# Kernel tuning notes

Hardware: AMD Instinct MI355X
Metric: run time of the kernel (lower is better)

Reference implementation:

```python
import jax, jax.numpy as jnp
import numpy as np

N, E, G = 100000, 800000, 1
DV, DE, DU, H = 64, 32, 32, 128

def _w(key, shape):
    return jax.random.normal(key, shape, dtype=jnp.float32) * 0.05

def setup_inputs() -> dict:
    key = jax.random.key(0)
    ks = jax.random.split(key, 16)
    inp = {
        "node_attr": jax.random.normal(ks[0], (N, DV), dtype=jnp.float32),
        "edges": jax.random.randint(ks[1], (2, E), 0, N, dtype=jnp.int64 if jax.config.jax_enable_x64 else jnp.int32),
        "edge_attr": jax.random.normal(ks[2], (E, DE), dtype=jnp.float32),
        "u": jax.random.normal(ks[3], (G, DU), dtype=jnp.float32),
        "node_idx": jnp.zeros((N,), dtype=jnp.int32),
        "edge_idx": jnp.zeros((E,), dtype=jnp.int32),
        # edge MLP: concat(src, dst, edge_attr, u) -> H -> H
        "W1e": _w(ks[4], (2 * DV + DE + DU, H)), "b1e": jnp.zeros((H,), jnp.float32),
        "W2e": _w(ks[5], (H, H)), "b2e": jnp.zeros((H,), jnp.float32),
        # node MLP: concat(node_attr, aggregated_edges, u) -> H -> H
        "W1n": _w(ks[6], (DV + H + DU, H)), "b1n": jnp.zeros((H,), jnp.float32),
        "W2n": _w(ks[7], (H, H)), "b2n": jnp.zeros((H,), jnp.float32),
        # global MLP: concat(node_mean, edge_mean, u) -> H -> H
        "W1g": _w(ks[8], (H + H + DU, H)), "b1g": jnp.zeros((H,), jnp.float32),
        "W2g": _w(ks[9], (H, H)), "b2g": jnp.zeros((H,), jnp.float32),
    }
    return inp

def _mlp(x, W1, b1, W2, b2):
    return jax.nn.relu(x @ W1 + b1) @ W2 + b2

def _seg_mean(x, seg, num):
    s = jax.ops.segment_sum(x, seg, num_segments=num)
    c = jax.ops.segment_sum(jnp.ones((x.shape[0], 1), x.dtype), seg, num_segments=num)
    return s / jnp.maximum(c, 1.0)

def reference(node_attr, edges, edge_attr, u, node_idx, edge_idx,
              W1e, b1e, W2e, b2e, W1n, b1n, W2n, b2n, W1g, b1g, W2g, b2g):
    row, col = edges[0], edges[1]
    # edge model: gather endpoint features, concat with edge/global attrs
    e_in = jnp.concatenate([node_attr[row], node_attr[col], edge_attr, u[edge_idx]], axis=-1)
    e = _mlp(e_in, W1e, b1e, W2e, b2e)                        # [E, H]
    # node model: scatter-add incoming edge messages onto receivers (col)
    agg = jax.ops.segment_sum(e, col, num_segments=node_attr.shape[0])  # [N, H]
    v_in = jnp.concatenate([node_attr, agg, u[node_idx]], axis=-1)
    v = _mlp(v_in, W1n, b1n, W2n, b2n)                        # [N, H]
    # global model: per-graph mean pooling of nodes and edges
    nv = _seg_mean(v, node_idx, u.shape[0])                   # [G, H]
    ne = _seg_mean(e, edge_idx, u.shape[0])                   # [G, H]
    g_in = jnp.concatenate([nv, ne, u], axis=-1)
    g = _mlp(g_in, W1g, b1g, W2g, b2g)                        # [G, H]
    return v, e, g
```

## Files before the change

### kernel.cpp

```cpp
#include <hip/hip_runtime.h>

#define N_NODES 100000
#define N_EDGES 800000
#define DV 64
#define DE 32
#define DU 32
#define H 128

#define NTILES_E (N_EDGES / 64)

typedef short bf16x8 __attribute__((ext_vector_type(8)));
typedef unsigned short u16;
typedef u16 u16x8 __attribute__((ext_vector_type(8)));
typedef float f32x4 __attribute__((ext_vector_type(4)));

#define OFF_ESUM 0
#define OFF_VSUM 8192
#define OFF_BIAS 16384
#define OFF_PART 17408
#define OFF_WBUF 19456
#define OFF_DEG  175104
#define OFF_OFFS 575104
#define OFF_BUCK 975104

#define W1ET_OFF 0
#define W2ET_OFF 20480
#define W1NT_OFF 36864
#define W2NT_OFF 61440
#define WBUF_ELEMS 77824

#define NPART 391

__device__ inline u16 f2bf(float x) {
  union { float f; unsigned u; } c; c.f = x;
  unsigned r = c.u + 0x7FFFu + ((c.u >> 16) & 1u);
  return (u16)(r >> 16);
}

__global__ void prep_weights(const float* __restrict__ W1e, const float* __restrict__ W2e,
                             const float* __restrict__ W1n, const float* __restrict__ W2n,
                             u16* __restrict__ wbuf) {
  int i = blockIdx.x * blockDim.x + threadIdx.x;
  if (i < 20480) {
    int j = i / 160, k = i - j * 160;
    wbuf[W1ET_OFF + i] = f2bf(W1e[k * H + j]);
  } else if (i < 36864) {
    int t = i - 20480; int j = t >> 7, k = t & 127;
    wbuf[i] = f2bf(W2e[k * H + j]);
  } else if (i < 61440) {
    int t = i - 36864; int j = t / 192, k = t - j * 192;
    wbuf[i] = f2bf(W1n[k * H + j]);
  } else if (i < WBUF_ELEMS) {
    int t = i - 61440; int j = t >> 7, k = t & 127;
    wbuf[i] = f2bf(W2n[k * H + j]);
  }
}

__global__ void prep_bias(const float* __restrict__ uattr,
                          const float* __restrict__ W1e, const float* __restrict__ b1e,
                          const float* __restrict__ W1n, const float* __restrict__ b1n,
                          float* __restrict__ bias) {
  int t = threadIdx.x;
  float be = b1e[t];
  float bn = b1n[t];
  for (int k = 0; k < DU; ++k) {
    float uk = uattr[k];
    be += uk * W1e[(2 * DV + DE + k) * H + t];
    bn += uk * W1n[(DV + H + k) * H + t];
  }
  bias[t] = be;
  bias[128 + t] = bn;
}

__global__ void degree_kernel(const int* __restrict__ edges, int* __restrict__ deg) {
  int i = blockIdx.x * 256 + threadIdx.x;
  if (i < N_EDGES) atomicAdd(&deg[edges[N_EDGES + i]], 1);
}

__global__ void scan_part(const int* __restrict__ deg, int* __restrict__ part) {
  int i = blockIdx.x * 256 + threadIdx.x;
  int v = (i < N_NODES) ? deg[i] : 0;
#pragma unroll
  for (int m = 1; m < 64; m <<= 1) v += __shfl_xor(v, m);
  __shared__ int s[4];
  if ((threadIdx.x & 63) == 0) s[threadIdx.x >> 6] = v;
  __syncthreads();
  if (threadIdx.x == 0) part[blockIdx.x] = s[0] + s[1] + s[2] + s[3];
}

__global__ void scan_top(int* __restrict__ part) {
  __shared__ int s[512];
  int t = threadIdx.x;
  s[t] = (t < NPART) ? part[t] : 0;
  __syncthreads();
  for (int d = 1; d < 512; d <<= 1) {
    int v = (t >= d) ? s[t - d] : 0;
    __syncthreads();
    s[t] += v;
    __syncthreads();
  }
  if (t < NPART) part[t] = (t == 0) ? 0 : s[t - 1];
}

__global__ void scan_down(const int* __restrict__ part, int* __restrict__ deg_cursor,
                          int* __restrict__ offsets) {
  __shared__ int s[256];
  int b = blockIdx.x, t = threadIdx.x;
  int i = b * 256 + t;
  int v = (i < N_NODES) ? deg_cursor[i] : 0;
  s[t] = v;
  __syncthreads();
  for (int d = 1; d < 256; d <<= 1) {
    int u = (t >= d) ? s[t - d] : 0;
    __syncthreads();
    s[t] += u;
    __syncthreads();
  }
  int excl = s[t] - v + part[b];
  if (i < N_NODES) { offsets[i] = excl; deg_cursor[i] = excl; }
}

__global__ void fill_kernel(const int* __restrict__ edges, int* __restrict__ cursor,
                            int* __restrict__ bucket) {
  int i = blockIdx.x * 256 + threadIdx.x;
  if (i < N_EDGES) {
    int d = edges[N_EDGES + i];
    int pos = atomicAdd(&cursor[d], 1);
    bucket[pos] = i;
  }
}

__global__ __launch_bounds__(256, 3) void edge_kernel(
    const float* __restrict__ node_attr, const int* __restrict__ edges,
    const float* __restrict__ edge_attr,
    const u16* __restrict__ wbuf, const float* __restrict__ bias_f,
    const float* __restrict__ b2,
    float* __restrict__ e_out, float* __restrict__ esum_p)
{
  __shared__ __align__(16) u16 Hs[64][132];

  const int tid = threadIdx.x;
  const int wave = tid >> 6, lane = tid & 63;
  const int l15 = lane & 15, lg = lane >> 4;
  const int kc = lg * 8;
  const int wc = wave * 32;
  const long e0 = (long)blockIdx.x * 64;

  bf16x8 w1[5][2];
  {
    const u16* w1t = wbuf + W1ET_OFF;
#pragma unroll
    for (int cf = 0; cf < 2; ++cf) {
      const u16* p1 = w1t + (wc + cf * 16 + l15) * 160 + kc;
#pragma unroll
      for (int ks = 0; ks < 5; ++ks) w1[ks][cf] = *(const bf16x8*)(p1 + ks * 32);
    }
  }
  float bias1[2] = { bias_f[wc + l15], bias_f[wc + 16 + l15] };

  int sid[4], did[4];
#pragma unroll
  for (int rf = 0; rf < 4; ++rf) {
    sid[rf] = edges[e0 + rf * 16 + l15];
    did[rf] = edges[(long)N_EDGES + e0 + rf * 16 + l15];
  }

  f32x4 acc[4][2];
#pragma unroll
  for (int rf = 0; rf < 4; ++rf)
#pragma unroll
    for (int cf = 0; cf < 2; ++cf)
#pragma unroll
      for (int j = 0; j < 4; ++j) acc[rf][cf][j] = 0.f;

#pragma unroll
  for (int ks = 0; ks < 5; ++ks) {
    f32x4 ga[4], gb[4];
#pragma unroll
    for (int rf = 0; rf < 4; ++rf) {
      const float* p;
      if (ks == 0)      p = node_attr + (long)sid[rf] * DV + kc;
      else if (ks == 1) p = node_attr + (long)sid[rf] * DV + 32 + kc;
      else if (ks == 2) p = node_attr + (long)did[rf] * DV + kc;
      else if (ks == 3) p = node_attr + (long)did[rf] * DV + 32 + kc;
      else              p = edge_attr + (e0 + rf * 16 + l15) * DE + kc;
      ga[rf] = *(const f32x4*)p;
      gb[rf] = *(const f32x4*)(p + 4);
    }
#pragma unroll
    for (int rf = 0; rf < 4; ++rf) {
      u16x8 a;
      a[0] = f2bf(ga[rf][0]); a[1] = f2bf(ga[rf][1]);
      a[2] = f2bf(ga[rf][2]); a[3] = f2bf(ga[rf][3]);
      a[4] = f2bf(gb[rf][0]); a[5] = f2bf(gb[rf][1]);
      a[6] = f2bf(gb[rf][2]); a[7] = f2bf(gb[rf][3]);
      acc[rf][0] = __builtin_amdgcn_mfma_f32_16x16x32_bf16((bf16x8)a, w1[ks][0], acc[rf][0], 0, 0, 0);
      acc[rf][1] = __builtin_amdgcn_mfma_f32_16x16x32_bf16((bf16x8)a, w1[ks][1], acc[rf][1], 0, 0, 0);
    }
  }

#pragma unroll
  for (int rf = 0; rf < 4; ++rf)
#pragma unroll
    for (int cf = 0; cf < 2; ++cf)
#pragma unroll
      for (int j = 0; j < 4; ++j) {
        float hv = acc[rf][cf][j] + bias1[cf];
        hv = hv > 0.f ? hv : 0.f;
        Hs[rf * 16 + lg * 4 + j][wc + cf * 16 + l15] = f2bf(hv);
      }

  bf16x8 w2[4][2];
  {
    const u16* w2t = wbuf + W2ET_OFF;
#pragma unroll
    for (int cf = 0; cf < 2; ++cf) {
      const u16* p2 = w2t + (wc + cf * 16 + l15) * 128 + kc;
#pragma unroll
      for (int ks = 0; ks < 4; ++ks) w2[ks][cf] = *(const bf16x8*)(p2 + ks * 32);
    }
  }
  float bias2[2] = { b2[wc + l15], b2[wc + 16 + l15] };

  __syncthreads();

#pragma unroll
  for (int rf = 0; rf < 4; ++rf)
#pragma unroll
    for (int cf = 0; cf < 2; ++cf)
#pragma unroll
      for (int j = 0; j < 4; ++j) acc[rf][cf][j] = 0.f;

#pragma unroll
  for (int ks = 0; ks < 4; ++ks) {
#pragma unroll
    for (int rf = 0; rf < 4; ++rf) {
      bf16x8 a = *(const bf16x8*)&Hs[rf * 16 + l15][ks * 32 + kc];
      acc[rf][0] = __builtin_amdgcn_mfma_f32_16x16x32_bf16(a, w2[ks][0], acc[rf][0], 0, 0, 0);
      acc[rf][1] = __builtin_amdgcn_mfma_f32_16x16x32_bf16(a, w2[ks][1], acc[rf][1], 0, 0, 0);
    }
  }

  float es0 = 0.f, es1 = 0.f;
#pragma unroll
  for (int rf = 0; rf < 4; ++rf) {
#pragma unroll
    for (int cf = 0; cf < 2; ++cf) {
      int colg = wc + cf * 16 + l15;
#pragma unroll
      for (int j = 0; j < 4; ++j) {
        float v = acc[rf][cf][j] + bias2[cf];
        long r = rf * 16 + lg * 4 + j;
        e_out[(e0 + r) * H + colg] = v;
        if (cf == 0) es0 += v; else es1 += v;
      }
    }
  }

#pragma unroll
  for (int m = 16; m < 64; m <<= 1) { es0 += __shfl_xor(es0, m); es1 += __shfl_xor(es1, m); }
  if (lane < 16) {
    atomicAdd(&esum_p[(wc + lane) * 16], es0);
    atomicAdd(&esum_p[(wc + 16 + lane) * 16], es1);
  }
}

__global__ __launch_bounds__(512, 2) void node_kernel(
    const float* __restrict__ node_attr, const u16* __restrict__ wbuf,
    const float* __restrict__ bias_f, const float* __restrict__ b2,
    const float* __restrict__ e_out, const int* __restrict__ offsets,
    const int* __restrict__ cursor, const int* __restrict__ bucket,
    float* __restrict__ v_out, float* __restrict__ vsum_p)
{
  __shared__ __align__(16) u16 X[64][196];
  __shared__ __align__(16) u16 Hs[64][132];

  const int tid = threadIdx.x;
  const int wave = tid >> 6, lane = tid & 63;
  const int l15 = lane & 15, lg = lane >> 4;
  const int wc = (wave & 3) * 32;
  const int rh = (wave >> 2) * 32;
  const long n0 = (long)blockIdx.x * 64;

  {
    int gr = tid >> 3, gs = tid & 7;
    long gn = n0 + gr; if (gn >= N_NODES) gn = N_NODES - 1;
    float a[16];
#pragma unroll
    for (int k = 0; k < 16; ++k) a[k] = 0.f;
    int s = offsets[gn], e = cursor[gn];
    int i = s;
    for (; i + 2 <= e; i += 2) {
      const float* p0 = e_out + (long)bucket[i] * H + gs * 16;
      const float* p1 = e_out + (long)bucket[i + 1] * H + gs * 16;
      float4 f0[4], f1[4];
#pragma unroll
      for (int k = 0; k < 4; ++k) f0[k] = *(const float4*)(p0 + k * 4);
#pragma unroll
      for (int k = 0; k < 4; ++k) f1[k] = *(const float4*)(p1 + k * 4);
#pragma unroll
      for (int k = 0; k < 4; ++k) {
        a[k * 4 + 0] += f0[k].x + f1[k].x;
        a[k * 4 + 1] += f0[k].y + f1[k].y;
        a[k * 4 + 2] += f0[k].z + f1[k].z;
        a[k * 4 + 3] += f0[k].w + f1[k].w;
      }
    }
    if (i < e) {
      const float* p0 = e_out + (long)bucket[i] * H + gs * 16;
#pragma unroll
      for (int k = 0; k < 4; ++k) {
        float4 f = *(const float4*)(p0 + k * 4);
        a[k * 4 + 0] += f.x; a[k * 4 + 1] += f.y;
        a[k * 4 + 2] += f.z; a[k * 4 + 3] += f.w;
      }
    }
#pragma unroll
    for (int k = 0; k < 2; ++k) {
      u16x8 pk;
#pragma unroll
      for (int j = 0; j < 8; ++j) pk[j] = f2bf(a[k * 8 + j]);
      *(u16x8*)&X[gr][64 + gs * 16 + k * 8] = pk;
    }
  }

  {
    int r = tid >> 3, col = (tid & 7) * 8;
    long n = n0 + r; if (n >= N_NODES) n = N_NODES - 1;
    const float* src = node_attr + n * DV + col;
    float4 f0 = *(const float4*)src;
    float4 f1 = *(const float4*)(src + 4);
    u16x8 p;
    p[0] = f2bf(f0.x); p[1] = f2bf(f0.y); p[2] = f2bf(f0.z); p[3] = f2bf(f0.w);
    p[4] = f2bf(f1.x); p[5] = f2bf(f1.y); p[6] = f2bf(f1.z); p[7] = f2bf(f1.w);
    *(u16x8*)&X[r][col] = p;
  }

  bf16x8 w1[6][2], w2[4][2];
  {
    const u16* w1t = wbuf + W1NT_OFF;
    const u16* w2t = wbuf + W2NT_OFF;
#pragma unroll
    for (int cf = 0; cf < 2; ++cf) {
      const u16* p1 = w1t + (wc + cf * 16 + l15) * 192 + lg * 8;
#pragma unroll
      for (int ks = 0; ks < 6; ++ks) w1[ks][cf] = *(const bf16x8*)(p1 + ks * 32);
      const u16* p2 = w2t + (wc + cf * 16 + l15) * 128 + lg * 8;
#pragma unroll
      for (int ks = 0; ks < 4; ++ks) w2[ks][cf] = *(const bf16x8*)(p2 + ks * 32);
    }
  }

  __syncthreads();

  f32x4 acc[2][2];
#pragma unroll
  for (int rf = 0; rf < 2; ++rf)
#pragma unroll
    for (int cf = 0; cf < 2; ++cf)
#pragma unroll
      for (int j = 0; j < 4; ++j) acc[rf][cf][j] = 0.f;

#pragma unroll
  for (int ks = 0; ks < 6; ++ks) {
#pragma unroll
    for (int rf = 0; rf < 2; ++rf) {
      bf16x8 a = *(const bf16x8*)&X[rh + rf * 16 + l15][ks * 32 + lg * 8];
      acc[rf][0] = __builtin_amdgcn_mfma_f32_16x16x32_bf16(a, w1[ks][0], acc[rf][0], 0, 0, 0);
      acc[rf][1] = __builtin_amdgcn_mfma_f32_16x16x32_bf16(a, w1[ks][1], acc[rf][1], 0, 0, 0);
    }
  }

  float bias1[2] = { bias_f[128 + wc + l15], bias_f[128 + wc + 16 + l15] };
#pragma unroll
  for (int rf = 0; rf < 2; ++rf)
#pragma unroll
    for (int cf = 0; cf < 2; ++cf)
#pragma unroll
      for (int j = 0; j < 4; ++j) {
        float hv = acc[rf][cf][j] + bias1[cf];
        hv = hv > 0.f ? hv : 0.f;
        Hs[rh + rf * 16 + lg * 4 + j][wc + cf * 16 + l15] = f2bf(hv);
      }

  __syncthreads();

#pragma unroll
  for (int rf = 0; rf < 2; ++rf)
#pragma unroll
    for (int cf = 0; cf < 2; ++cf)
#pragma unroll
      for (int j = 0; j < 4; ++j) acc[rf][cf][j] = 0.f;

#pragma unroll
  for (int ks = 0; ks < 4; ++ks) {
#pragma unroll
    for (int rf = 0; rf < 2; ++rf) {
      bf16x8 a = *(const bf16x8*)&Hs[rh + rf * 16 + l15][ks * 32 + lg * 8];
      acc[rf][0] = __builtin_amdgcn_mfma_f32_16x16x32_bf16(a, w2[ks][0], acc[rf][0], 0, 0, 0);
      acc[rf][1] = __builtin_amdgcn_mfma_f32_16x16x32_bf16(a, w2[ks][1], acc[rf][1], 0, 0, 0);
    }
  }

  float bias2[2] = { b2[wc + l15], b2[wc + 16 + l15] };
  float vs0 = 0.f, vs1 = 0.f;
#pragma unroll
  for (int rf = 0; rf < 2; ++rf) {
#pragma unroll
    for (int cf = 0; cf < 2; ++cf) {
      int colg = wc + cf * 16 + l15;
#pragma unroll
      for (int j = 0; j < 4; ++j) {
        int r = rh + rf * 16 + lg * 4 + j;
        long n = n0 + r;
        if (n < N_NODES) {
          float v = acc[rf][cf][j] + bias2[cf];
          v_out[n * H + colg] = v;
          if (cf == 0) vs0 += v; else vs1 += v;
        }
      }
    }
  }
#pragma unroll
  for (int m = 16; m < 64; m <<= 1) { vs0 += __shfl_xor(vs0, m); vs1 += __shfl_xor(vs1, m); }
  if (lane < 16) {
    atomicAdd(&vsum_p[(wc + lane) * 16], vs0);
    atomicAdd(&vsum_p[(wc + 16 + lane) * 16], vs1);
  }
}

__global__ void global_kernel(const float* __restrict__ uattr,
    const float* __restrict__ W1g, const float* __restrict__ b1g,
    const float* __restrict__ W2g, const float* __restrict__ b2g,
    const float* __restrict__ esum_p, const float* __restrict__ vsum_p,
    float* __restrict__ g_out)
{
  __shared__ float gin[288];
  __shared__ float hbuf[128];
  int t = threadIdx.x;
  gin[t]       = vsum_p[t * 16] * (1.f / (float)N_NODES);
  gin[128 + t] = esum_p[t * 16] * (1.f / (float)N_EDGES);
  if (t < 32) gin[256 + t] = uattr[t];
  __syncthreads();
  float a = b1g[t];
  for (int k = 0; k < 288; ++k) a += gin[k] * W1g[k * H + t];
  hbuf[t] = fmaxf(a, 0.f);
  __syncthreads();
  float b = b2g[t];
  for (int k = 0; k < 128; ++k) b += hbuf[k] * W2g[k * H + t];
  g_out[t] = b;
}

extern "C" void kernel_launch(void* const* d_in, const int* in_sizes, int n_in,
                              void* d_out, int out_size, void* d_ws, size_t ws_size,
                              hipStream_t stream) {
  const float* node_attr = (const float*)d_in[0];
  const int*   edges     = (const int*)d_in[1];
  const float* edge_attr = (const float*)d_in[2];
  const float* uattr     = (const float*)d_in[3];
  const float* W1e = (const float*)d_in[6];  const float* b1e = (const float*)d_in[7];
  const float* W2e = (const float*)d_in[8];  const float* b2e = (const float*)d_in[9];
  const float* W1n = (const float*)d_in[10]; const float* b1n = (const float*)d_in[11];
  const float* W2n = (const float*)d_in[12]; const float* b2n = (const float*)d_in[13];
  const float* W1g = (const float*)d_in[14]; const float* b1g = (const float*)d_in[15];
  const float* W2g = (const float*)d_in[16]; const float* b2g = (const float*)d_in[17];

  float* out   = (float*)d_out;
  float* v_out = out;
  float* e_out = out + (long)N_NODES * H;
  float* g_out = out + (long)N_NODES * H + (long)N_EDGES * H;

  char* ws = (char*)d_ws;
  float* esum_p = (float*)(ws + OFF_ESUM);
  float* vsum_p = (float*)(ws + OFF_VSUM);
  float* bias_f = (float*)(ws + OFF_BIAS);
  int*   part   = (int*)(ws + OFF_PART);
  u16*   wbuf   = (u16*)(ws + OFF_WBUF);
  int*   deg    = (int*)(ws + OFF_DEG);
  int*   offs   = (int*)(ws + OFF_OFFS);
  int*   buck   = (int*)(ws + OFF_BUCK);

  hipMemsetAsync(ws, 0, 16384, stream);
  hipMemsetAsync(deg, 0, N_NODES * sizeof(int), stream);

  prep_weights<<<WBUF_ELEMS / 256, 256, 0, stream>>>(W1e, W2e, W1n, W2n, wbuf);
  prep_bias<<<1, 128, 0, stream>>>(uattr, W1e, b1e, W1n, b1n, bias_f);
  degree_kernel<<<(N_EDGES + 255) / 256, 256, 0, stream>>>(edges, deg);
  scan_part<<<NPART, 256, 0, stream>>>(deg, part);
  scan_top<<<1, 512, 0, stream>>>(part);
  scan_down<<<NPART, 256, 0, stream>>>(part, deg, offs);
  fill_kernel<<<(N_EDGES + 255) / 256, 256, 0, stream>>>(edges, deg, buck);

  edge_kernel<<<NTILES_E, 256, 0, stream>>>(node_attr, edges, edge_attr, wbuf,
                                            bias_f, b2e, e_out, esum_p);
  node_kernel<<<(N_NODES + 63) / 64, 512, 0, stream>>>(node_attr, wbuf,
                                                       bias_f, b2n,
                                                       e_out, offs, deg, buck,
                                                       v_out, vsum_p);
  global_kernel<<<1, 128, 0, stream>>>(uattr, W1g, b1g, W2g, b2g, esum_p, vsum_p, g_out);
}
```

Before: 666.9 us.

## Give each wave its own edge tile, stage outputs, and move edge-sum to node kernel

The edge kernel now has each wave process an independent 16-edge tile across all 128 output columns. This removes the block-wide __syncthreads and the split of columns across waves. Weights are read per MFMA from global/L2 instead of being held in registers. Outputs are staged through per-wave LDS so the e_out stores become coalesced float4 writes. The global edge-sum atomics are dropped from the edge kernel and rebuilt in the node kernel from the per-node aggregates it already gathers, which relies on every edge being bucketed to some node.

```diff
diff --git a/kernel.cpp b/kernel.cpp
--- a/kernel.cpp
+++ b/kernel.cpp
@@ -6,8 +6,6 @@
 #define DE 32
 #define DU 32
 #define H 128
-
-#define NTILES_E (N_EDGES / 64)
 
 typedef short bf16x8 __attribute__((ext_vector_type(8)));
 typedef unsigned short u16;
@@ -134,134 +132,96 @@
     const float* __restrict__ node_attr, const int* __restrict__ edges,
     const float* __restrict__ edge_attr,
     const u16* __restrict__ wbuf, const float* __restrict__ bias_f,
-    const float* __restrict__ b2,
-    float* __restrict__ e_out, float* __restrict__ esum_p)
+    const float* __restrict__ b2, float* __restrict__ e_out)
 {
-  __shared__ __align__(16) u16 Hs[64][132];
+  __shared__ __align__(16) char smem[33792];
 
   const int tid = threadIdx.x;
   const int wave = tid >> 6, lane = tid & 63;
   const int l15 = lane & 15, lg = lane >> 4;
   const int kc = lg * 8;
-  const int wc = wave * 32;
-  const long e0 = (long)blockIdx.x * 64;
-
-  bf16x8 w1[5][2];
-  {
-    const u16* w1t = wbuf + W1ET_OFF;
-#pragma unroll
-    for (int cf = 0; cf < 2; ++cf) {
-      const u16* p1 = w1t + (wc + cf * 16 + l15) * 160 + kc;
-#pragma unroll
-      for (int ks = 0; ks < 5; ++ks) w1[ks][cf] = *(const bf16x8*)(p1 + ks * 32);
-    }
-  }
-  float bias1[2] = { bias_f[wc + l15], bias_f[wc + 16 + l15] };
-
-  int sid[4], did[4];
-#pragma unroll
-  for (int rf = 0; rf < 4; ++rf) {
-    sid[rf] = edges[e0 + rf * 16 + l15];
-    did[rf] = edges[(long)N_EDGES + e0 + rf * 16 + l15];
-  }
-
-  f32x4 acc[4][2];
-#pragma unroll
-  for (int rf = 0; rf < 4; ++rf)
-#pragma unroll
-    for (int cf = 0; cf < 2; ++cf)
-#pragma unroll
-      for (int j = 0; j < 4; ++j) acc[rf][cf][j] = 0.f;
-
+  char* wsm = smem + wave * 8448;
+  u16 (*Hs)[136]   = (u16(*)[136])wsm;
+  float (*OT)[132] = (float(*)[132])wsm;
+
+  const long e0 = ((long)blockIdx.x * 4 + wave) * 16;
+
+  const int sid = edges[e0 + l15];
+  const int did = edges[(long)N_EDGES + e0 + l15];
+
+  f32x4 g[5][2];
 #pragma unroll
   for (int ks = 0; ks < 5; ++ks) {
-    f32x4 ga[4], gb[4];
-#pragma unroll
-    for (int rf = 0; rf < 4; ++rf) {
-      const float* p;
-      if (ks == 0)      p = node_attr + (long)sid[rf] * DV + kc;
-      else if (ks == 1) p = node_attr + (long)sid[rf] * DV + 32 + kc;
-      else if (ks == 2) p = node_attr + (long)did[rf] * DV + kc;
-      else if (ks == 3) p = node_attr + (long)did[rf] * DV + 32 + kc;
-      else              p = edge_attr + (e0 + rf * 16 + l15) * DE + kc;
-      ga[rf] = *(const f32x4*)p;
-      gb[rf] = *(const f32x4*)(p + 4);
-    }
-#pragma unroll
-    for (int rf = 0; rf < 4; ++rf) {
-      u16x8 a;
-      a[0] = f2bf(ga[rf][0]); a[1] = f2bf(ga[rf][1]);
-      a[2] = f2bf(ga[rf][2]); a[3] = f2bf(ga[rf][3]);
-      a[4] = f2bf(gb[rf][0]); a[5] = f2bf(gb[rf][1]);
-      a[6] = f2bf(gb[rf][2]); a[7] = f2bf(gb[rf][3]);
-      acc[rf][0] = __builtin_amdgcn_mfma_f32_16x16x32_bf16((bf16x8)a, w1[ks][0], acc[rf][0], 0, 0, 0);
-      acc[rf][1] = __builtin_amdgcn_mfma_f32_16x16x32_bf16((bf16x8)a, w1[ks][1], acc[rf][1], 0, 0, 0);
-    }
-  }
-
-#pragma unroll
-  for (int rf = 0; rf < 4; ++rf)
-#pragma unroll
-    for (int cf = 0; cf < 2; ++cf)
-#pragma unroll
-      for (int j = 0; j < 4; ++j) {
-        float hv = acc[rf][cf][j] + bias1[cf];
-        hv = hv > 0.f ? hv : 0.f;
-        Hs[rf * 16 + lg * 4 + j][wc + cf * 16 + l15] = f2bf(hv);
-      }
-
-  bf16x8 w2[4][2];
-  {
-    const u16* w2t = wbuf + W2ET_OFF;
-#pragma unroll
-    for (int cf = 0; cf < 2; ++cf) {
-      const u16* p2 = w2t + (wc + cf * 16 + l15) * 128 + kc;
-#pragma unroll
-      for (int ks = 0; ks < 4; ++ks) w2[ks][cf] = *(const bf16x8*)(p2 + ks * 32);
-    }
-  }
-  float bias2[2] = { b2[wc + l15], b2[wc + 16 + l15] };
-
-  __syncthreads();
-
-#pragma unroll
-  for (int rf = 0; rf < 4; ++rf)
-#pragma unroll
-    for (int cf = 0; cf < 2; ++cf)
-#pragma unroll
-      for (int j = 0; j < 4; ++j) acc[rf][cf][j] = 0.f;
-
+    const float* p;
+    if (ks < 2)      p = node_attr + (long)sid * DV + ks * 32 + kc;
+    else if (ks < 4) p = node_attr + (long)did * DV + (ks - 2) * 32 + kc;
+    else             p = edge_attr + (e0 + l15) * DE + kc;
+    g[ks][0] = *(const f32x4*)p;
+    g[ks][1] = *(const f32x4*)(p + 4);
+  }
+
+  f32x4 acc[8];
+#pragma unroll
+  for (int cf = 0; cf < 8; ++cf)
+#pragma unroll
+    for (int j = 0; j < 4; ++j) acc[cf][j] = 0.f;
+
+  const u16* w1t = wbuf + W1ET_OFF;
+#pragma unroll
+  for (int ks = 0; ks < 5; ++ks) {
+    u16x8 a;
+    a[0] = f2bf(g[ks][0][0]); a[1] = f2bf(g[ks][0][1]);
+    a[2] = f2bf(g[ks][0][2]); a[3] = f2bf(g[ks][0][3]);
+    a[4] = f2bf(g[ks][1][0]); a[5] = f2bf(g[ks][1][1]);
+    a[6] = f2bf(g[ks][1][2]); a[7] = f2bf(g[ks][1][3]);
+#pragma unroll
+    for (int cf = 0; cf < 8; ++cf) {
+      bf16x8 w = *(const bf16x8*)(w1t + (cf * 16 + l15) * 160 + ks * 32 + kc);
+      acc[cf] = __builtin_amdgcn_mfma_f32_16x16x32_bf16((bf16x8)a, w, acc[cf], 0, 0, 0);
+    }
+  }
+
+#pragma unroll
+  for (int cf = 0; cf < 8; ++cf) {
+    float b1v = bias_f[cf * 16 + l15];
+#pragma unroll
+    for (int j = 0; j < 4; ++j) {
+      float hv = acc[cf][j] + b1v;
+      hv = hv > 0.f ? hv : 0.f;
+      Hs[lg * 4 + j][cf * 16 + l15] = f2bf(hv);
+    }
+  }
+
+#pragma unroll
+  for (int cf = 0; cf < 8; ++cf)
+#pragma unroll
+    for (int j = 0; j < 4; ++j) acc[cf][j] = 0.f;
+
+  const u16* w2t = wbuf + W2ET_OFF;
 #pragma unroll
   for (int ks = 0; ks < 4; ++ks) {
-#pragma unroll
-    for (int rf = 0; rf < 4; ++rf) {
-      bf16x8 a = *(const bf16x8*)&Hs[rf * 16 + l15][ks * 32 + kc];
-      acc[rf][0] = __builtin_amdgcn_mfma_f32_16x16x32_bf16(a, w2[ks][0], acc[rf][0], 0, 0, 0);
-      acc[rf][1] = __builtin_amdgcn_mfma_f32_16x16x32_bf16(a, w2[ks][1], acc[rf][1], 0, 0, 0);
-    }
-  }
-
-  float es0 = 0.f, es1 = 0.f;
-#pragma unroll
-  for (int rf = 0; rf < 4; ++rf) {
-#pragma unroll
-    for (int cf = 0; cf < 2; ++cf) {
-      int colg = wc + cf * 16 + l15;
-#pragma unroll
-      for (int j = 0; j < 4; ++j) {
-        float v = acc[rf][cf][j] + bias2[cf];
-        long r = rf * 16 + lg * 4 + j;
-        e_out[(e0 + r) * H + colg] = v;
-        if (cf == 0) es0 += v; else es1 += v;
-      }
-    }
-  }
-
-#pragma unroll
-  for (int m = 16; m < 64; m <<= 1) { es0 += __shfl_xor(es0, m); es1 += __shfl_xor(es1, m); }
-  if (lane < 16) {
-    atomicAdd(&esum_p[(wc + lane) * 16], es0);
-    atomicAdd(&esum_p[(wc + 16 + lane) * 16], es1);
+    bf16x8 a = *(const bf16x8*)&Hs[l15][ks * 32 + kc];
+#pragma unroll
+    for (int cf = 0; cf < 8; ++cf) {
+      bf16x8 w = *(const bf16x8*)(w2t + (cf * 16 + l15) * 128 + ks * 32 + kc);
+      acc[cf] = __builtin_amdgcn_mfma_f32_16x16x32_bf16(a, w, acc[cf], 0, 0, 0);
+    }
+  }
+
+#pragma unroll
+  for (int cf = 0; cf < 8; ++cf) {
+    float b2v = b2[cf * 16 + l15];
+#pragma unroll
+    for (int j = 0; j < 4; ++j)
+      OT[lg * 4 + j][cf * 16 + l15] = acc[cf][j] + b2v;
+  }
+
+#pragma unroll
+  for (int i = 0; i < 8; ++i) {
+    int ch = lane + i * 64;
+    int r = ch >> 5, c4 = ch & 31;
+    f32x4 f = *(const f32x4*)&OT[r][c4 * 4];
+    *(f32x4*)(e_out + (e0 + r) * H + c4 * 4) = f;
   }
 }
 
@@ -270,10 +230,12 @@
     const float* __restrict__ bias_f, const float* __restrict__ b2,
     const float* __restrict__ e_out, const int* __restrict__ offsets,
     const int* __restrict__ cursor, const int* __restrict__ bucket,
-    float* __restrict__ v_out, float* __restrict__ vsum_p)
+    float* __restrict__ v_out, float* __restrict__ vsum_p,
+    float* __restrict__ esum_p)
 {
   __shared__ __align__(16) u16 X[64][196];
   __shared__ __align__(16) u16 Hs[64][132];
+  __shared__ float esw[8][8][16];
 
   const int tid = threadIdx.x;
   const int wave = tid >> 6, lane = tid & 63;
@@ -284,7 +246,9 @@
 
   {
     int gr = tid >> 3, gs = tid & 7;
-    long gn = n0 + gr; if (gn >= N_NODES) gn = N_NODES - 1;
+    long gn = n0 + gr;
+    bool valid = (gn < N_NODES);
+    if (!valid) gn = N_NODES - 1;
     float a[16];
 #pragma unroll
     for (int k = 0; k < 16; ++k) a[k] = 0.f;
@@ -313,6 +277,19 @@
         float4 f = *(const float4*)(p0 + k * 4);
         a[k * 4 + 0] += f.x; a[k * 4 + 1] += f.y;
         a[k * 4 + 2] += f.z; a[k * 4 + 3] += f.w;
+      }
+    }
+    {
+      float es[16];
+#pragma unroll
+      for (int k = 0; k < 16; ++k) es[k] = valid ? a[k] : 0.f;
+#pragma unroll
+      for (int m = 8; m <= 32; m <<= 1)
+#pragma unroll
+        for (int k = 0; k < 16; ++k) es[k] += __shfl_xor(es[k], m);
+      if (lane < 8) {
+#pragma unroll
+        for (int k = 0; k < 16; ++k) esw[wave][lane][k] = es[k];
       }
     }
 #pragma unroll
@@ -352,6 +329,14 @@
   }
 
   __syncthreads();
+
+  if (tid < 128) {
+    int gs = tid >> 4, k = tid & 15;
+    float s = 0.f;
+#pragma unroll
+    for (int w = 0; w < 8; ++w) s += esw[w][gs][k];
+    atomicAdd(&esum_p[tid * 16], s);
+  }
 
   f32x4 acc[2][2];
 #pragma unroll
@@ -491,11 +476,11 @@
   scan_down<<<NPART, 256, 0, stream>>>(part, deg, offs);
   fill_kernel<<<(N_EDGES + 255) / 256, 256, 0, stream>>>(edges, deg, buck);
 
-  edge_kernel<<<NTILES_E, 256, 0, stream>>>(node_attr, edges, edge_attr, wbuf,
-                                            bias_f, b2e, e_out, esum_p);
+  edge_kernel<<<N_EDGES / 64, 256, 0, stream>>>(node_attr, edges, edge_attr, wbuf,
+                                                bias_f, b2e, e_out);
   node_kernel<<<(N_NODES + 63) / 64, 512, 0, stream>>>(node_attr, wbuf,
                                                        bias_f, b2n,
                                                        e_out, offs, deg, buck,
-                                                       v_out, vsum_p);
+                                                       v_out, vsum_p, esum_p);
   global_kernel<<<1, 128, 0, stream>>>(uattr, W1g, b1g, W2g, b2g, esum_p, vsum_p, g_out);
 }
```

New measurement: 678.5 us. No clear change (+1.7%).
